# Kernel tuning notes

Hardware: AMD Instinct MI355X
Metric: run time of the kernel (lower is better)

## Reference

```python
import jax, jax.numpy as jnp
import numpy as np

B, T, D = 8, 2048, 1024
E, S = 8, 1            # num_experts, num_slots
FF = 4 * (S * D)       # ffn_mult * (num_slots * hiddens)

def setup_inputs() -> dict:
    key = jax.random.key(0)
    ks = jax.random.split(key, 7)
    sd = S * D
    inp = {
        "X":  jax.random.normal(ks[0], (B, T, D), dtype=jnp.float32),
        # slots gating MLP (single linear D -> E*S)
        "Wg": jax.random.normal(ks[1], (D, E * S), dtype=jnp.float32) / np.sqrt(D),
        "bg": jnp.zeros((E * S,), dtype=jnp.float32),
        # expert FFN (weights SHARED across experts, as in source [FFN(...)]*E)
        "W1": jax.random.normal(ks[2], (sd, FF), dtype=jnp.float32) / np.sqrt(sd),
        "b1": jnp.zeros((FF,), dtype=jnp.float32),
        "W2": jax.random.normal(ks[3], (FF, sd), dtype=jnp.float32) / np.sqrt(FF),
        "b2": jnp.zeros((sd,), dtype=jnp.float32),
    }
    return inp

def reference(X, Wg, bg, W1, b1, W2, b2):
    # logits: (B, T, E*S)
    logits = jnp.einsum('btd,de->bte', X, Wg) + bg
    dispatch_w = jax.nn.softmax(logits, axis=1)   # over tokens T
    combine_w = jax.nn.softmax(logits, axis=2)    # over slots E*S
    # slots = dispatch_w^T @ X : (B, E*S, D) -> (B, E, S*D)
    slots = jnp.einsum('bte,btd->bed', dispatch_w, X).reshape(B, E, S * D)
    # shared-weight FFN applied per expert slot (dropout=0 at eval)
    h = jax.nn.silu(jnp.einsum('bef,fh->beh', slots, W1) + b1)
    y = jnp.einsum('beh,hf->bef', h, W2) + b2     # (B, E, S*D)
    y = y.reshape(B, E * S, D)
    # combine: (B, T, E*S) @ (B, E*S, D)
    return jnp.einsum('bte,bed->btd', combine_w, y)
```

## Files before the change

### kernel.cpp

```cpp
#include <hip/hip_runtime.h>
#include <math.h>

#define B_  8
#define T_  2048
#define D_  1024
#define E_  8
#define FF_ 4096
#define N_  64
#define BT_ (B_*T_)

__global__ __launch_bounds__(256) void k_logits_part(
    const float* __restrict__ X, const float* __restrict__ Wg,
    float* __restrict__ part)
{
    __shared__ float wgT[E_ * 128];
    __shared__ float xt[256 * 36];

    const int tid = threadIdx.x;
    const int bt0 = blockIdx.x * 256;
    const int d0  = blockIdx.y * 128;

    #pragma unroll
    for (int r = 0; r < 4; ++r) {
        int idx = r * 256 + tid;
        wgT[(idx & 7) * 128 + (idx >> 3)] = Wg[(size_t)d0 * E_ + idx];
    }

    float acc[8];
    #pragma unroll
    for (int e = 0; e < 8; ++e) acc[e] = 0.f;

    for (int dt = 0; dt < 4; ++dt) {
        __syncthreads();
        #pragma unroll
        for (int r = 0; r < 8; ++r) {
            int fi = r * 256 + tid;
            int token = fi >> 3, dj = fi & 7;
            const float4 v = *(const float4*)
                &X[(size_t)(bt0 + token) * D_ + d0 + dt * 32 + dj * 4];
            *(float4*)&xt[token * 36 + dj * 4] = v;
        }
        __syncthreads();
        #pragma unroll
        for (int dj = 0; dj < 8; ++dj) {
            const float4 x4 = *(const float4*)&xt[tid * 36 + dj * 4];
            #pragma unroll
            for (int e = 0; e < 8; ++e) {
                const float4 w4 = *(const float4*)&wgT[e * 128 + dt * 32 + dj * 4];
                acc[e] += x4.x * w4.x + x4.y * w4.y + x4.z * w4.z + x4.w * w4.w;
            }
        }
    }

    float* pp = &part[(size_t)blockIdx.y * BT_ * E_ + (size_t)(bt0 + tid) * E_];
    *(float4*)&pp[0] = make_float4(acc[0], acc[1], acc[2], acc[3]);
    *(float4*)&pp[4] = make_float4(acc[4], acc[5], acc[6], acc[7]);
}

__global__ __launch_bounds__(256) void k_logits_merge(
    const float* __restrict__ part, const float* __restrict__ bg,
    float* __restrict__ logits, float* __restrict__ sumexp)
{
    __shared__ float red[8 * 256];
    const int tid = threadIdx.x;
    const int token = blockIdx.x * 256 + tid;
    const int b = blockIdx.x >> 3;

    float a[8];
    #pragma unroll
    for (int e = 0; e < 8; ++e) a[e] = 0.f;
    #pragma unroll
    for (int p = 0; p < 8; ++p) {
        const float* pp = &part[(size_t)p * BT_ * E_ + (size_t)token * E_];
        const float4 v0 = *(const float4*)&pp[0];
        const float4 v1 = *(const float4*)&pp[4];
        a[0] += v0.x; a[1] += v0.y; a[2] += v0.z; a[3] += v0.w;
        a[4] += v1.x; a[5] += v1.y; a[6] += v1.z; a[7] += v1.w;
    }
    #pragma unroll
    for (int e = 0; e < 8; ++e) a[e] += bg[e];

    float* lp = &logits[(size_t)token * E_];
    *(float4*)&lp[0] = make_float4(a[0], a[1], a[2], a[3]);
    *(float4*)&lp[4] = make_float4(a[4], a[5], a[6], a[7]);

    #pragma unroll
    for (int e = 0; e < 8; ++e) red[e * 256 + tid] = expf(a[e]);
    __syncthreads();
    for (int s = 128; s >= 1; s >>= 1) {
        if (tid < s) {
            #pragma unroll
            for (int e = 0; e < 8; ++e)
                red[e * 256 + tid] += red[e * 256 + tid + s];
        }
        __syncthreads();
    }
    if (tid < 8) atomicAdd(&sumexp[b * E_ + tid], red[tid * 256]);
}

__global__ __launch_bounds__(256) void k_slots_part(
    const float* __restrict__ X, const float* __restrict__ logits,
    const float* __restrict__ sumexp, float* __restrict__ part)
{
    __shared__ float wlds[32 * 8];
    const int tid = threadIdx.x;
    const int ts = blockIdx.x, b = blockIdx.y;
    const int t0 = ts * 32;

    {
        int t = tid >> 3, e = tid & 7;
        wlds[tid] = expf(logits[((size_t)b * T_ + t0 + t) * E_ + e])
                    / sumexp[b * E_ + e];
    }
    __syncthreads();

    float4 acc[8];
    #pragma unroll
    for (int e = 0; e < 8; ++e) { acc[e].x = acc[e].y = acc[e].z = acc[e].w = 0.f; }

    const float* xb = &X[((size_t)b * T_ + t0) * D_ + tid * 4];
    #pragma unroll 8
    for (int t = 0; t < 32; ++t) {
        const float4 x4 = *(const float4*)&xb[(size_t)t * D_];
        const float4 wA = *(const float4*)&wlds[t * 8];
        const float4 wB = *(const float4*)&wlds[t * 8 + 4];
        const float w[8] = {wA.x, wA.y, wA.z, wA.w, wB.x, wB.y, wB.z, wB.w};
        #pragma unroll
        for (int e = 0; e < 8; ++e) {
            acc[e].x += x4.x * w[e];
            acc[e].y += x4.y * w[e];
            acc[e].z += x4.z * w[e];
            acc[e].w += x4.w * w[e];
        }
    }
    #pragma unroll
    for (int e = 0; e < 8; ++e) {
        *(float4*)&part[(size_t)ts * (N_ * D_) + (size_t)(b * E_ + e) * D_ + tid * 4] = acc[e];
    }
}

__global__ __launch_bounds__(256) void k_reduce_slots(
    const float* __restrict__ part, float* __restrict__ slots)
{
    const int i = blockIdx.x * 256 + threadIdx.x;
    float s = 0.f;
    #pragma unroll
    for (int p = 0; p < 64; ++p) s += part[(size_t)p * (N_ * D_) + i];
    slots[i] = s;
}

__global__ __launch_bounds__(256) void k_gemm_part(
    const float* __restrict__ A, const float* __restrict__ W,
    float* __restrict__ part, int K, int F)
{
    __shared__ float As[64][64];

    const int tid = threadIdx.x;
    const int rg  = tid >> 5;
    const int cg  = tid & 31;
    const int f0  = blockIdx.x * 128 + cg * 4;
    const int k0  = blockIdx.y * 64;

    #pragma unroll
    for (int i = 0; i < 4; ++i) {
        int idx = i * 256 + tid;
        int row = idx >> 4, kq = idx & 15;
        const float4 v = *(const float4*)&A[(size_t)row * K + k0 + kq * 4];
        *(float4*)&As[row][kq * 4] = v;
    }
    __syncthreads();

    float4 acc[8];
    #pragma unroll
    for (int r = 0; r < 8; ++r) { acc[r].x = acc[r].y = acc[r].z = acc[r].w = 0.f; }

    #pragma unroll 2
    for (int kq = 0; kq < 16; ++kq) {
        float4 w0 = *(const float4*)&W[(size_t)(k0 + kq * 4 + 0) * F + f0];
        float4 w1 = *(const float4*)&W[(size_t)(k0 + kq * 4 + 1) * F + f0];
        float4 w2 = *(const float4*)&W[(size_t)(k0 + kq * 4 + 2) * F + f0];
        float4 w3 = *(const float4*)&W[(size_t)(k0 + kq * 4 + 3) * F + f0];
        #pragma unroll
        for (int r = 0; r < 8; ++r) {
            const float4 a = *(const float4*)&As[rg * 8 + r][kq * 4];
            acc[r].x += a.x * w0.x + a.y * w1.x + a.z * w2.x + a.w * w3.x;
            acc[r].y += a.x * w0.y + a.y * w1.y + a.z * w2.y + a.w * w3.y;
            acc[r].z += a.x * w0.z + a.y * w1.z + a.z * w2.z + a.w * w3.z;
            acc[r].w += a.x * w0.w + a.y * w1.w + a.z * w2.w + a.w * w3.w;
        }
    }

    float* pb = &part[(size_t)blockIdx.y * N_ * F];
    #pragma unroll
    for (int r = 0; r < 8; ++r)
        *(float4*)&pb[(size_t)(rg * 8 + r) * F + f0] = acc[r];
}

__global__ __launch_bounds__(256) void k_reduce_silu(
    const float* __restrict__ part, const float* __restrict__ b1,
    float* __restrict__ h)
{
    const int i = blockIdx.x * 256 + threadIdx.x;
    float s = 0.f;
    #pragma unroll
    for (int p = 0; p < 16; ++p) s += part[(size_t)p * (N_ * FF_) + i];
    s += b1[i & (FF_ - 1)];
    h[i] = s / (1.f + expf(-s));
}

__global__ __launch_bounds__(256) void k_reduce_bias(
    const float* __restrict__ part, const float* __restrict__ b2,
    float* __restrict__ y)
{
    const int i = blockIdx.x * 256 + threadIdx.x;
    float s = 0.f;
    #pragma unroll
    for (int p = 0; p < 64; ++p) s += part[(size_t)p * (N_ * D_) + i];
    y[i] = s + b2[i & (D_ - 1)];
}

__global__ __launch_bounds__(256) void k_combine(
    const float* __restrict__ logits, const float* __restrict__ y,
    float* __restrict__ out)
{
    __shared__ float wlds[64 * 8];
    const int tid = threadIdx.x;
    const int dc = blockIdx.x, tc = blockIdx.y, b = blockIdx.z;
    const int t0 = tc * 64;

    if (tid < 64) {
        const float* lp = &logits[((size_t)b * T_ + t0 + tid) * E_];
        float ex[8]; float s = 0.f;
        #pragma unroll
        for (int i = 0; i < 8; ++i) { ex[i] = expf(lp[i]); s += ex[i]; }
        const float invs = 1.f / s;
        #pragma unroll
        for (int i = 0; i < 8; ++i) wlds[tid * 8 + i] = ex[i] * invs;
    }
    __syncthreads();

    const int d = dc * 256 + tid;
    float yv[8];
    #pragma unroll
    for (int e = 0; e < 8; ++e) yv[e] = y[(size_t)(b * E_ + e) * D_ + d];

    for (int t = 0; t < 64; ++t) {
        const float4 wA = *(const float4*)&wlds[t * 8];
        const float4 wB = *(const float4*)&wlds[t * 8 + 4];
        const float acc = wA.x * yv[0] + wA.y * yv[1] + wA.z * yv[2] + wA.w * yv[3]
                        + wB.x * yv[4] + wB.y * yv[5] + wB.z * yv[6] + wB.w * yv[7];
        out[((size_t)b * T_ + t0 + t) * D_ + d] = acc;
    }
}

extern "C" void kernel_launch(void* const* d_in, const int* in_sizes, int n_in,
                              void* d_out, int out_size, void* d_ws, size_t ws_size,
                              hipStream_t stream)
{
    const float* X  = (const float*)d_in[0];
    const float* Wg = (const float*)d_in[1];
    const float* bg = (const float*)d_in[2];
    const float* W1 = (const float*)d_in[3];
    const float* b1 = (const float*)d_in[4];
    const float* W2 = (const float*)d_in[5];
    const float* b2 = (const float*)d_in[6];
    float* out = (float*)d_out;

    float* wsf    = (float*)d_ws;
    float* logits = wsf;
    float* sumexp = logits + BT_ * E_;
    float* slots  = sumexp + 64;
    float* h      = slots + N_ * D_;
    float* y      = h + N_ * FF_;

    float* part = out;

    hipMemsetAsync(sumexp, 0, 64 * sizeof(float), stream);

    hipLaunchKernelGGL(k_logits_part,  dim3(BT_ / 256, 8), dim3(256), 0, stream,
                       X, Wg, part);
    hipLaunchKernelGGL(k_logits_merge, dim3(BT_ / 256),    dim3(256), 0, stream,
                       part, bg, logits, sumexp);
    hipLaunchKernelGGL(k_slots_part,   dim3(64, 8),        dim3(256), 0, stream,
                       X, logits, sumexp, part);
    hipLaunchKernelGGL(k_reduce_slots, dim3(256),          dim3(256), 0, stream,
                       part, slots);
    hipLaunchKernelGGL(k_gemm_part,    dim3(FF_ / 128, 1024 / 64), dim3(256), 0, stream,
                       slots, W1, part, 1024, FF_);
    hipLaunchKernelGGL(k_reduce_silu,  dim3(N_ * FF_ / 256), dim3(256), 0, stream,
                       part, b1, h);
    hipLaunchKernelGGL(k_gemm_part,    dim3(D_ / 128, FF_ / 64), dim3(256), 0, stream,
                       h, W2, part, FF_, D_);
    hipLaunchKernelGGL(k_reduce_bias,  dim3(N_ * D_ / 256), dim3(256), 0, stream,
                       part, b2, y);
    hipLaunchKernelGGL(k_combine,      dim3(4, 32, 8), dim3(256), 0, stream,
                       logits, y, out);
}
```

Measured before the change: 260.4 us.

## Drop memset and atomics, read Wg directly, halve split-K partial counts

The logits kernel now reads the gating weights straight from global memory, so the per-block LDS transpose and one barrier are gone. The softmax-over-tokens denominators are no longer accumulated with atomics into a memset buffer. Each merge block writes its own per-block partial sum, and the slots kernel reduces those partials itself. The slots kernel and both FFN split-K GEMMs process twice as many tokens or K rows per block, which halves the partial buffers the reduction kernels must read, at the cost of fewer blocks and less parallelism.

Measured after the change: 251.3 us. 3.5% less time.

```diff
diff --git a/kernel.cpp b/kernel.cpp
--- a/kernel.cpp
+++ b/kernel.cpp
@@ -13,25 +13,18 @@
     const float* __restrict__ X, const float* __restrict__ Wg,
     float* __restrict__ part)
 {
-    __shared__ float wgT[E_ * 128];
     __shared__ float xt[256 * 36];
 
     const int tid = threadIdx.x;
     const int bt0 = blockIdx.x * 256;
     const int d0  = blockIdx.y * 128;
 
-    #pragma unroll
-    for (int r = 0; r < 4; ++r) {
-        int idx = r * 256 + tid;
-        wgT[(idx & 7) * 128 + (idx >> 3)] = Wg[(size_t)d0 * E_ + idx];
-    }
-
     float acc[8];
     #pragma unroll
     for (int e = 0; e < 8; ++e) acc[e] = 0.f;
 
     for (int dt = 0; dt < 4; ++dt) {
-        __syncthreads();
+        if (dt) __syncthreads();
         #pragma unroll
         for (int r = 0; r < 8; ++r) {
             int fi = r * 256 + tid;
@@ -44,10 +37,16 @@
         #pragma unroll
         for (int dj = 0; dj < 8; ++dj) {
             const float4 x4 = *(const float4*)&xt[tid * 36 + dj * 4];
+            const int db = d0 + dt * 32 + dj * 4;
+            const float xv[4] = {x4.x, x4.y, x4.z, x4.w};
             #pragma unroll
-            for (int e = 0; e < 8; ++e) {
-                const float4 w4 = *(const float4*)&wgT[e * 128 + dt * 32 + dj * 4];
-                acc[e] += x4.x * w4.x + x4.y * w4.y + x4.z * w4.z + x4.w * w4.w;
+            for (int r = 0; r < 4; ++r) {
+                const float4 wlo = *(const float4*)&Wg[(size_t)(db + r) * 8];
+                const float4 whi = *(const float4*)&Wg[(size_t)(db + r) * 8 + 4];
+                acc[0] += xv[r] * wlo.x; acc[1] += xv[r] * wlo.y;
+                acc[2] += xv[r] * wlo.z; acc[3] += xv[r] * wlo.w;
+                acc[4] += xv[r] * whi.x; acc[5] += xv[r] * whi.y;
+                acc[6] += xv[r] * whi.z; acc[7] += xv[r] * whi.w;
             }
         }
     }
@@ -59,12 +58,11 @@
 
 __global__ __launch_bounds__(256) void k_logits_merge(
     const float* __restrict__ part, const float* __restrict__ bg,
-    float* __restrict__ logits, float* __restrict__ sumexp)
+    float* __restrict__ logits, float* __restrict__ sexp_part)
 {
     __shared__ float red[8 * 256];
     const int tid = threadIdx.x;
     const int token = blockIdx.x * 256 + tid;
-    const int b = blockIdx.x >> 3;
 
     float a[8];
     #pragma unroll
@@ -95,22 +93,34 @@
         }
         __syncthreads();
     }
-    if (tid < 8) atomicAdd(&sumexp[b * E_ + tid], red[tid * 256]);
+    if (tid < 8) sexp_part[blockIdx.x * 8 + tid] = red[tid * 256];
 }
 
 __global__ __launch_bounds__(256) void k_slots_part(
     const float* __restrict__ X, const float* __restrict__ logits,
-    const float* __restrict__ sumexp, float* __restrict__ part)
-{
-    __shared__ float wlds[32 * 8];
+    const float* __restrict__ sexp_part, float* __restrict__ part)
+{
+    __shared__ float wlds[64 * 8];
+    __shared__ float red[64];
+    __shared__ float inv[8];
+
     const int tid = threadIdx.x;
     const int ts = blockIdx.x, b = blockIdx.y;
-    const int t0 = ts * 32;
-
-    {
-        int t = tid >> 3, e = tid & 7;
-        wlds[tid] = expf(logits[((size_t)b * T_ + t0 + t) * E_ + e])
-                    / sumexp[b * E_ + e];
+    const int t0 = ts * 64;
+
+    if (tid < 64) red[tid] = sexp_part[b * 64 + tid];
+    __syncthreads();
+    if (tid < 8) {
+        float s = 0.f;
+        #pragma unroll
+        for (int i = 0; i < 8; ++i) s += red[i * 8 + tid];
+        inv[tid] = 1.f / s;
+    }
+    __syncthreads();
+    #pragma unroll
+    for (int r = 0; r < 2; ++r) {
+        int idx = r * 256 + tid;
+        wlds[idx] = expf(logits[((size_t)b * T_ + t0) * E_ + idx]) * inv[idx & 7];
     }
     __syncthreads();
 
@@ -120,7 +130,7 @@
 
     const float* xb = &X[((size_t)b * T_ + t0) * D_ + tid * 4];
     #pragma unroll 8
-    for (int t = 0; t < 32; ++t) {
+    for (int t = 0; t < 64; ++t) {
         const float4 x4 = *(const float4*)&xb[(size_t)t * D_];
         const float4 wA = *(const float4*)&wlds[t * 8];
         const float4 wB = *(const float4*)&wlds[t * 8 + 4];
@@ -145,7 +155,7 @@
     const int i = blockIdx.x * 256 + threadIdx.x;
     float s = 0.f;
     #pragma unroll
-    for (int p = 0; p < 64; ++p) s += part[(size_t)p * (N_ * D_) + i];
+    for (int p = 0; p < 32; ++p) s += part[(size_t)p * (N_ * D_) + i];
     slots[i] = s;
 }
 
@@ -153,18 +163,18 @@
     const float* __restrict__ A, const float* __restrict__ W,
     float* __restrict__ part, int K, int F)
 {
-    __shared__ float As[64][64];
+    __shared__ float As[64][128];
 
     const int tid = threadIdx.x;
     const int rg  = tid >> 5;
     const int cg  = tid & 31;
     const int f0  = blockIdx.x * 128 + cg * 4;
-    const int k0  = blockIdx.y * 64;
-
-    #pragma unroll
-    for (int i = 0; i < 4; ++i) {
+    const int k0  = blockIdx.y * 128;
+
+    #pragma unroll
+    for (int i = 0; i < 8; ++i) {
         int idx = i * 256 + tid;
-        int row = idx >> 4, kq = idx & 15;
+        int row = idx >> 5, kq = idx & 31;
         const float4 v = *(const float4*)&A[(size_t)row * K + k0 + kq * 4];
         *(float4*)&As[row][kq * 4] = v;
     }
@@ -175,7 +185,7 @@
     for (int r = 0; r < 8; ++r) { acc[r].x = acc[r].y = acc[r].z = acc[r].w = 0.f; }
 
     #pragma unroll 2
-    for (int kq = 0; kq < 16; ++kq) {
+    for (int kq = 0; kq < 32; ++kq) {
         float4 w0 = *(const float4*)&W[(size_t)(k0 + kq * 4 + 0) * F + f0];
         float4 w1 = *(const float4*)&W[(size_t)(k0 + kq * 4 + 1) * F + f0];
         float4 w2 = *(const float4*)&W[(size_t)(k0 + kq * 4 + 2) * F + f0];
@@ -203,7 +213,7 @@
     const int i = blockIdx.x * 256 + threadIdx.x;
     float s = 0.f;
     #pragma unroll
-    for (int p = 0; p < 16; ++p) s += part[(size_t)p * (N_ * FF_) + i];
+    for (int p = 0; p < 8; ++p) s += part[(size_t)p * (N_ * FF_) + i];
     s += b1[i & (FF_ - 1)];
     h[i] = s / (1.f + expf(-s));
 }
@@ -215,7 +225,7 @@
     const int i = blockIdx.x * 256 + threadIdx.x;
     float s = 0.f;
     #pragma unroll
-    for (int p = 0; p < 64; ++p) s += part[(size_t)p * (N_ * D_) + i];
+    for (int p = 0; p < 32; ++p) s += part[(size_t)p * (N_ * D_) + i];
     y[i] = s + b2[i & (D_ - 1)];
 }
 
@@ -266,30 +276,28 @@
     const float* b2 = (const float*)d_in[6];
     float* out = (float*)d_out;
 
-    float* wsf    = (float*)d_ws;
-    float* logits = wsf;
-    float* sumexp = logits + BT_ * E_;
-    float* slots  = sumexp + 64;
-    float* h      = slots + N_ * D_;
-    float* y      = h + N_ * FF_;
+    float* wsf       = (float*)d_ws;
+    float* logits    = wsf;
+    float* sexp_part = logits + BT_ * E_;
+    float* slots     = sexp_part + 512;
+    float* h         = slots + N_ * D_;
+    float* y         = h + N_ * FF_;
 
     float* part = out;
-
-    hipMemsetAsync(sumexp, 0, 64 * sizeof(float), stream);
 
     hipLaunchKernelGGL(k_logits_part,  dim3(BT_ / 256, 8), dim3(256), 0, stream,
                        X, Wg, part);
     hipLaunchKernelGGL(k_logits_merge, dim3(BT_ / 256),    dim3(256), 0, stream,
-                       part, bg, logits, sumexp);
-    hipLaunchKernelGGL(k_slots_part,   dim3(64, 8),        dim3(256), 0, stream,
-                       X, logits, sumexp, part);
+                       part, bg, logits, sexp_part);
+    hipLaunchKernelGGL(k_slots_part,   dim3(32, 8),        dim3(256), 0, stream,
+                       X, logits, sexp_part, part);
     hipLaunchKernelGGL(k_reduce_slots, dim3(256),          dim3(256), 0, stream,
                        part, slots);
-    hipLaunchKernelGGL(k_gemm_part,    dim3(FF_ / 128, 1024 / 64), dim3(256), 0, stream,
+    hipLaunchKernelGGL(k_gemm_part,    dim3(FF_ / 128, 1024 / 128), dim3(256), 0, stream,
                        slots, W1, part, 1024, FF_);
     hipLaunchKernelGGL(k_reduce_silu,  dim3(N_ * FF_ / 256), dim3(256), 0, stream,
                        part, b1, h);
-    hipLaunchKernelGGL(k_gemm_part,    dim3(D_ / 128, FF_ / 64), dim3(256), 0, stream,
+    hipLaunchKernelGGL(k_gemm_part,    dim3(D_ / 128, FF_ / 128), dim3(256), 0, stream,
                        h, W2, part, FF_, D_);
     hipLaunchKernelGGL(k_reduce_bias,  dim3(N_ * D_ / 256), dim3(256), 0, stream,
                        part, b2, y);
```
